# Performance work log

Hardware: AMD Instinct MI355X
Metric: run time of the kernel (lower is better)

The kernel has to match this reference:

```python
import jax, jax.numpy as jnp
import numpy as np

B, S, HID = 2, 2048, 1024
H, D = 16, HID // 16  # heads, head_dim
ROPE_BASE = 10000.0


def setup_inputs() -> dict:
    key = jax.random.key(0)
    k1, k2, k3, k4 = jax.random.split(key, 4)
    scale = 1.0 / np.sqrt(HID)
    return {
        "hidden_states": jax.random.normal(k1, (B, S, HID), dtype=jnp.float32),
        "attention_mask": jnp.zeros((B, 1, 1, S), dtype=jnp.float32),
        "Wq": jax.random.normal(k2, (HID, HID), dtype=jnp.float32) * scale,
        "Wk": jax.random.normal(k3, (HID, HID), dtype=jnp.float32) * scale,
        "Wv": jax.random.normal(k4, (HID, HID), dtype=jnp.float32) * scale,
    }


def _rope_cos_sin(seq_len, dim, dtype):
    inv_freq = 1.0 / (ROPE_BASE ** (jnp.arange(0, dim, 2, dtype=jnp.float32) / dim))
    freqs = jnp.arange(seq_len, dtype=jnp.float32)[:, None] * inv_freq[None, :]  # (S, D/2)
    emb = jnp.concatenate([freqs, freqs], axis=-1)  # (S, D)
    return jnp.cos(emb).astype(dtype), jnp.sin(emb).astype(dtype)


def _rotate_half(x):
    x1, x2 = jnp.split(x, 2, axis=-1)
    return jnp.concatenate([-x2, x1], axis=-1)


def reference(hidden_states, attention_mask, Wq, Wk, Wv):
    b, s, _ = hidden_states.shape
    # QKV projections (no bias), split into heads: (b, H, s, D)
    def proj(W):
        return jnp.einsum('bse,de->bsd', hidden_states, W).reshape(b, s, H, D).transpose(0, 2, 1, 3)
    q, k, v = proj(Wq), proj(Wk), proj(Wv)
    # Rotary embedding on q, k over sequence positions
    cos, sin = _rope_cos_sin(s, D, hidden_states.dtype)  # (s, D)
    cos = cos[None, None]  # (1,1,s,D)
    sin = sin[None, None]
    q = q * cos + _rotate_half(q) * sin
    k = k * cos + _rotate_half(k) * sin
    # Scaled dot-product attention with additive mask
    scores = jnp.einsum('bhqd,bhkd->bhqk', q, k) / jnp.sqrt(jnp.asarray(D, hidden_states.dtype))
    scores = scores + attention_mask
    probs = jax.nn.softmax(scores, axis=-1)  # dropout p=0 (eval) -> identity
    ctx = jnp.einsum('bhqk,bhkd->bhqd', probs, v)
    return ctx.transpose(0, 2, 1, 3).reshape(b, s, H * D)
```

## Files before the change

### kernel.cpp

```cpp
#include <hip/hip_runtime.h>
#include <stdint.h>

typedef unsigned short u16;
typedef short bf16x8 __attribute__((ext_vector_type(8)));
typedef float f32x4 __attribute__((ext_vector_type(4)));

#define S_ 2048
#define HID_ 1024
#define H_ 16
#define D_ 64

#define LOG2E 1.4426950408889634f
#define SCALE_LOG2 0.18033688011112042f
#define MAXC_LOG2 11.541560327111707f

__device__ __forceinline__ u16 f2bf(float f) {
  uint32_t x = __builtin_bit_cast(uint32_t, f);
  uint32_t r = (x + 0x7fffu + ((x >> 16) & 1u)) >> 16;
  return (u16)r;
}
__device__ __forceinline__ uint32_t packbf2(float a, float b) {
  return (uint32_t)f2bf(a) | ((uint32_t)f2bf(b) << 16);
}
__device__ __forceinline__ uint32_t permpack(float a, float b) {
  return __builtin_amdgcn_perm(__builtin_bit_cast(uint32_t, b),
                               __builtin_bit_cast(uint32_t, a), 0x07060302u);
}

__device__ __forceinline__ void gl2lds16(const void* g, void* l) {
  __builtin_amdgcn_global_load_lds(
      (const __attribute__((address_space(1))) unsigned int*)g,
      (__attribute__((address_space(3))) unsigned int*)l, 16, 0, 0);
}

#define NX_ (1 << 20)
#define NW_ (1 << 18)
#define NROPE_ 65536
__global__ void prep_kernel(const float* __restrict__ X, const float* __restrict__ Wq,
                            const float* __restrict__ Wk, const float* __restrict__ Wv,
                            const float* __restrict__ mask, u16* __restrict__ Xb,
                            u16* __restrict__ Wqb, u16* __restrict__ Wkb,
                            u16* __restrict__ Wvb, float* __restrict__ cos_t,
                            float* __restrict__ sin_t, float* __restrict__ mask2) {
  int i = blockIdx.x * 256 + threadIdx.x;
  if (i < NX_ + 3 * NW_) {
    const float* src;
    u16* dst;
    int off;
    if (i < NX_) {
      src = X; dst = Xb; off = i;
    } else if (i < NX_ + NW_) {
      src = Wq; dst = Wqb; off = i - NX_;
    } else if (i < NX_ + 2 * NW_) {
      src = Wk; dst = Wkb; off = i - NX_ - NW_;
    } else {
      src = Wv; dst = Wvb; off = i - NX_ - 2 * NW_;
    }
    float4 v = ((const float4*)src)[off];
    uint2 packed;
    packed.x = packbf2(v.x, v.y);
    packed.y = packbf2(v.z, v.w);
    ((uint2*)dst)[off] = packed;
  } else if (i < NX_ + 3 * NW_ + NROPE_) {
    int t = i - (NX_ + 3 * NW_);
    int s = t >> 5, j = t & 31;
    float invf = powf(10000.0f, -(float)j * (1.0f / 32.0f));
    float ang = (float)s * invf;
    cos_t[t] = cosf(ang);
    sin_t[t] = sinf(ang);
  } else {
    int t = i - (NX_ + 3 * NW_ + NROPE_);
    mask2[t] = fmaf(mask[t], LOG2E, -MAXC_LOG2);
  }
}

__global__ __launch_bounds__(512, 2) void qkv_gemm_kernel(
    const u16* __restrict__ X, const u16* __restrict__ Wq, const u16* __restrict__ Wk,
    const u16* __restrict__ Wv, const float* __restrict__ cos_t,
    const float* __restrict__ sin_t, u16* __restrict__ Q, u16* __restrict__ K,
    u16* __restrict__ Vt) {
  __shared__ char smem[131072];
  int tid = threadIdx.x;
  int lane = tid & 63, wave = tid >> 6;
  int wm = wave >> 2, wn = wave & 3;
  int quad = lane >> 4, l16 = lane & 15;
  int nbase = blockIdx.x * 128;
  int mbase = blockIdx.y * 128;

#define STAGE_ALL(k0, buf)                                                        \
  {                                                                               \
    _Pragma("unroll") for (int it = 0; it < 8; ++it) {                            \
      int j = (it & 1) * 512 + tid;                                               \
      int r = j >> 3, gs = j & 7, gsrc = gs ^ (r & 7);                            \
      const u16* src; int rb;                                                     \
      if ((it >> 1) == 0)      { src = X;  rb = mbase + r; }                      \
      else if ((it >> 1) == 1) { src = Wq; rb = nbase + r; }                      \
      else if ((it >> 1) == 2) { src = Wk; rb = nbase + r; }                      \
      else                     { src = Wv; rb = nbase + r; }                      \
      gl2lds16(src + (size_t)rb * HID_ + (k0) + gsrc * 8,                         \
               (buf) + (it >> 1) * 16384 + j * 16);                               \
    }                                                                             \
  }

  STAGE_ALL(0, smem)

  f32x4 acc[3][4][2] = {};

  for (int kk = 0; kk < 16; ++kk) {
    const char* buf = smem + (kk & 1) * 65536;
    __syncthreads();

    if (kk < 15)
      STAGE_ALL((kk + 1) * 64, smem + ((kk + 1) & 1) * 65536)

#pragma unroll
    for (int kh = 0; kh < 2; ++kh) {
      bf16x8 afrag[4];
#pragma unroll
      for (int i4 = 0; i4 < 4; ++i4) {
        int r = wm * 64 + i4 * 16 + l16;
        int L = r * 8 + ((kh * 4 + quad) ^ (r & 7));
        afrag[i4] = *(const bf16x8*)(buf + L * 16);
      }
#pragma unroll
      for (int w = 0; w < 3; ++w) {
        const char* Bs = buf + 16384 + w * 16384;
        bf16x8 bfrag[2];
#pragma unroll
        for (int j2 = 0; j2 < 2; ++j2) {
          int r = (wn >> 1) * 64 + (wn & 1) * 16 + j2 * 32 + l16;
          int L = r * 8 + ((kh * 4 + quad) ^ (r & 7));
          bfrag[j2] = *(const bf16x8*)(Bs + L * 16);
        }
        if (w == 2) {
#pragma unroll
          for (int i4 = 0; i4 < 4; ++i4)
#pragma unroll
            for (int j2 = 0; j2 < 2; ++j2)
              acc[2][i4][j2] = __builtin_amdgcn_mfma_f32_16x16x32_bf16(
                  afrag[i4], bfrag[j2], acc[2][i4][j2], 0, 0, 0);
        } else if (w == 1) {
#pragma unroll
          for (int i4 = 0; i4 < 4; ++i4)
#pragma unroll
            for (int j2 = 0; j2 < 2; ++j2)
              acc[1][i4][j2] = __builtin_amdgcn_mfma_f32_16x16x32_bf16(
                  bfrag[j2], afrag[i4], acc[1][i4][j2], 0, 0, 0);
        } else {
#pragma unroll
          for (int i4 = 0; i4 < 4; ++i4)
#pragma unroll
            for (int j2 = 0; j2 < 2; ++j2)
              acc[0][i4][j2] = __builtin_amdgcn_mfma_f32_16x16x32_bf16(
                  bfrag[j2], afrag[i4], acc[0][i4][j2], 0, 0, 0);
        }
      }
    }
  }
#undef STAGE_ALL

#pragma unroll
  for (int i4 = 0; i4 < 4; ++i4)
#pragma unroll
    for (int j2 = 0; j2 < 2; ++j2) {
      int m = mbase + wm * 64 + i4 * 16 + quad * 4;
      int n = nbase + (wn >> 1) * 64 + (wn & 1) * 16 + j2 * 32 + l16;
      int b = m >> 11, s0 = m & 2047;
      int h = n >> 6, d = n & 63;
      uint2 pk;
      pk.x = packbf2(acc[2][i4][j2][0], acc[2][i4][j2][1]);
      pk.y = packbf2(acc[2][i4][j2][2], acc[2][i4][j2][3]);
      *(uint2*)(Vt + (((size_t)(b * H_ + h)) * D_ + d) * S_ + s0) = pk;
    }

#pragma unroll
  for (int w = 0; w < 2; ++w) {
    u16* dst = (w == 0) ? Q : K;
#pragma unroll
    for (int i4 = 0; i4 < 4; ++i4) {
      int m = mbase + wm * 64 + i4 * 16 + l16;
      int n1 = nbase + (wn >> 1) * 64 + (wn & 1) * 16 + quad * 4;
      int b = m >> 11, s = m & 2047;
      int h = n1 >> 6, d1 = n1 & 63;
      float4 c4 = *(const float4*)(cos_t + s * 32 + d1);
      float4 s4 = *(const float4*)(sin_t + s * 32 + d1);
      float y1[4], y2[4];
#pragma unroll
      for (int r = 0; r < 4; ++r) {
        float cr = ((const float*)&c4)[r], sr = ((const float*)&s4)[r];
        float x1 = acc[w][i4][0][r], x2 = acc[w][i4][1][r];
        y1[r] = x1 * cr - x2 * sr;
        y2[r] = x2 * cr + x1 * sr;
      }
      size_t base = ((size_t)(b * H_ + h) * S_ + s) * D_;
      uint2 p1, p2;
      p1.x = packbf2(y1[0], y1[1]);
      p1.y = packbf2(y1[2], y1[3]);
      p2.x = packbf2(y2[0], y2[1]);
      p2.y = packbf2(y2[2], y2[3]);
      *(uint2*)(dst + base + d1) = p1;
      *(uint2*)(dst + base + d1 + 32) = p2;
    }
  }
}

__device__ __forceinline__ void softmax_pack(const f32x4 (*s)[4], const float4* mv,
                                             bf16x8 (*pp)[2]) {
#pragma unroll
  for (int qb = 0; qb < 2; ++qb) {
    uint32_t a[4][2];
#pragma unroll
    for (int jt = 0; jt < 4; ++jt) {
      float pf[4];
#pragma unroll
      for (int r = 0; r < 4; ++r) {
        float mvr = ((const float*)&mv[jt])[r];
        pf[r] = __builtin_amdgcn_exp2f(fmaf(s[qb][jt][r], SCALE_LOG2, mvr));
      }
      a[jt][0] = permpack(pf[0], pf[1]);
      a[jt][1] = permpack(pf[2], pf[3]);
    }
#pragma unroll
    for (int kh = 0; kh < 2; ++kh) {
      uint32_t tt[4];
#pragma unroll
      for (int i = 0; i < 2; ++i) {
        auto r1 = __builtin_amdgcn_permlane32_swap(a[2 * kh][i], a[2 * kh + 1][i],
                                                   false, false);
        auto r2 = __builtin_amdgcn_permlane16_swap(r1[0], r1[1], false, false);
        tt[i] = r2[0];
        tt[2 + i] = r2[1];
      }
      union { uint32_t u[4]; bf16x8 v; } cv;
      cv.u[0] = tt[0]; cv.u[1] = tt[1]; cv.u[2] = tt[2]; cv.u[3] = tt[3];
      pp[qb][kh] = cv.v;
    }
  }
}

__global__ __launch_bounds__(256, 2) void flash_kernel(
    const u16* __restrict__ Q, const u16* __restrict__ K, const u16* __restrict__ Vt,
    const float* __restrict__ mask2, float* __restrict__ out) {
  __shared__ char smem[49152];
  int tid = threadIdx.x, wave = tid >> 6;
  int lane = tid & 63;
  int quad = lane >> 4, l16 = lane & 15;
  int bh = blockIdx.y, b = bh >> 4, h = bh & 15;
  int qw = blockIdx.x * 128 + wave * 32;
  const u16* Kbase = K + (size_t)bh * S_ * D_;
  const u16* Vbase = Vt + (size_t)bh * D_ * S_;

  char* bk0 = smem + l16 * 128 + ((quad ^ (l16 & 7)) * 16);
  char* bk1 = smem + l16 * 128 + (((4 + quad) ^ (l16 & 7)) * 16);

  int r0 = tid >> 3, gs = tid & 7, gsrc = gs ^ (r0 & 7);
  size_t koff = (size_t)r0 * D_ + gsrc * 8;
  size_t voff = (size_t)r0 * S_ + gsrc * 8;
  const u16* kg = Kbase;
  const u16* vg = Vbase;
  const float* mq = mask2 + b * S_;

#define STAGE(SB)                                                      \
  {                                                                    \
    gl2lds16(kg + koff, smem + (SB) * 16384 + tid * 16);               \
    gl2lds16(kg + koff + 32 * D_, smem + (SB) * 16384 + 4096 + tid * 16); \
    gl2lds16(vg + voff, smem + (SB) * 16384 + 8192 + tid * 16);        \
    gl2lds16(vg + voff + 32 * S_, smem + (SB) * 16384 + 12288 + tid * 16); \
    kg += 64 * D_;                                                     \
    vg += 64;                                                          \
  }

#define MVLOAD                                                         \
  {                                                                    \
    _Pragma("unroll") for (int jt = 0; jt < 4; ++jt)                   \
        mv[jt] = *(const float4*)(mq + jt * 16 + quad * 4);            \
    mq += 64;                                                          \
  }

#define QK_Z(KOFF, s)                                                             \
  {                                                                               \
    _Pragma("unroll") for (int jt = 0; jt < 4; ++jt) {                            \
      bf16x8 kf0 = *(const bf16x8*)(bk0 + (KOFF) + jt * 2048);                    \
      bf16x8 kf1 = *(const bf16x8*)(bk1 + (KOFF) + jt * 2048);                    \
      s[0][jt] = __builtin_amdgcn_mfma_f32_16x16x32_bf16(kf0, qfrag[0][0], zc, 0, 0, 0); \
      s[0][jt] = __builtin_amdgcn_mfma_f32_16x16x32_bf16(kf1, qfrag[0][1], s[0][jt], 0, 0, 0); \
      s[1][jt] = __builtin_amdgcn_mfma_f32_16x16x32_bf16(kf0, qfrag[1][0], zc, 0, 0, 0); \
      s[1][jt] = __builtin_amdgcn_mfma_f32_16x16x32_bf16(kf1, qfrag[1][1], s[1][jt], 0, 0, 0); \
    }                                                                             \
  }

#define PV(VOFF)                                                                  \
  {                                                                               \
    lacc[0] = __builtin_amdgcn_mfma_f32_16x16x32_bf16(pp[0][0], ones, lacc[0], 0, 0, 0); \
    lacc[0] = __builtin_amdgcn_mfma_f32_16x16x32_bf16(pp[0][1], ones, lacc[0], 0, 0, 0); \
    lacc[1] = __builtin_amdgcn_mfma_f32_16x16x32_bf16(pp[1][0], ones, lacc[1], 0, 0, 0); \
    lacc[1] = __builtin_amdgcn_mfma_f32_16x16x32_bf16(pp[1][1], ones, lacc[1], 0, 0, 0); \
    _Pragma("unroll") for (int jd = 0; jd < 4; ++jd) {                            \
      bf16x8 vf0 = *(const bf16x8*)(bk0 + (VOFF) + jd * 2048);                    \
      bf16x8 vf1 = *(const bf16x8*)(bk1 + (VOFF) + jd * 2048);                    \
      o[0][jd] = __builtin_amdgcn_mfma_f32_16x16x32_bf16(pp[0][0], vf0, o[0][jd], 0, 0, 0); \
      o[0][jd] = __builtin_amdgcn_mfma_f32_16x16x32_bf16(pp[0][1], vf1, o[0][jd], 0, 0, 0); \
      o[1][jd] = __builtin_amdgcn_mfma_f32_16x16x32_bf16(pp[1][0], vf0, o[1][jd], 0, 0, 0); \
      o[1][jd] = __builtin_amdgcn_mfma_f32_16x16x32_bf16(pp[1][1], vf1, o[1][jd], 0, 0, 0); \
    }                                                                             \
  }

#define BODY(M)                                                        \
  {                                                                    \
    __syncthreads();                                                   \
    STAGE(((M) + 1) % 3)                                               \
    __builtin_amdgcn_s_setprio(1);                                     \
    PV((((M) + 2) % 3) * 16384 + 8192)                                 \
    f32x4 s[2][4];                                                     \
    QK_Z((M) * 16384, s)                                               \
    __builtin_amdgcn_s_setprio(0);                                     \
    softmax_pack(s, mv, pp);                                           \
    MVLOAD                                                             \
  }

  bf16x8 qfrag[2][2];
#pragma unroll
  for (int qb = 0; qb < 2; ++qb) {
    const u16* qp = Q + ((size_t)bh * S_ + qw + qb * 16 + l16) * D_ + quad * 8;
    qfrag[qb][0] = *(const bf16x8*)qp;
    qfrag[qb][1] = *(const bf16x8*)(qp + 32);
  }
  bf16x8 ones;
#pragma unroll
  for (int j = 0; j < 8; ++j) ones[j] = (short)0x3f80;
  const f32x4 zc = {0.f, 0.f, 0.f, 0.f};

  f32x4 o[2][4] = {};
  f32x4 lacc[2] = {};
  bf16x8 pp[2][2];
  float4 mv[4];

  STAGE(0)
  MVLOAD

  {
    __syncthreads();
    STAGE(1)
    f32x4 s[2][4];
    __builtin_amdgcn_s_setprio(1);
    QK_Z(0, s)
    __builtin_amdgcn_s_setprio(0);
    softmax_pack(s, mv, pp);
    MVLOAD
  }

  for (int j = 0; j < 10; ++j) {
    BODY(1)
    BODY(2)
    BODY(0)
  }

  {
    __syncthreads();
    __builtin_amdgcn_s_setprio(1);
    PV(0 * 16384 + 8192)
    f32x4 s[2][4];
    QK_Z(1 * 16384, s)
    __builtin_amdgcn_s_setprio(0);
    softmax_pack(s, mv, pp);
  }

  PV(1 * 16384 + 8192)

#undef STAGE
#undef MVLOAD
#undef QK_Z
#undef PV
#undef BODY

  float inv[2][4];
#pragma unroll
  for (int qb = 0; qb < 2; ++qb)
#pragma unroll
    for (int r = 0; r < 4; ++r) inv[qb][r] = 1.0f / lacc[qb][r];
#pragma unroll
  for (int qb = 0; qb < 2; ++qb)
#pragma unroll
    for (int jd = 0; jd < 4; ++jd) {
#pragma unroll
      for (int r = 0; r < 4; ++r) {
        int d = jd * 16 + l16;
        int q = qw + qb * 16 + quad * 4 + r;
        out[(((size_t)b * S_ + q) * H_ + h) * D_ + d] = o[qb][jd][r] * inv[qb][r];
      }
    }
}

extern "C" void kernel_launch(void* const* d_in, const int* in_sizes, int n_in,
                              void* d_out, int out_size, void* d_ws, size_t ws_size,
                              hipStream_t stream) {
  const float* hid = (const float*)d_in[0];
  const float* mask = (const float*)d_in[1];
  const float* Wq = (const float*)d_in[2];
  const float* Wk = (const float*)d_in[3];
  const float* Wv = (const float*)d_in[4];
  float* out = (float*)d_out;
  char* ws = (char*)d_ws;

  u16* Xbf = (u16*)ws;
  u16* Wqb = (u16*)(ws + (8u << 20));
  u16* Wkb = (u16*)(ws + (10u << 20));
  u16* Wvb = (u16*)(ws + (12u << 20));
  u16* Qb = (u16*)(ws + (14u << 20));
  u16* Kb = (u16*)(ws + (22u << 20));
  u16* Vtb = (u16*)(ws + (30u << 20));
  float* cos_t = (float*)(ws + (38u << 20));
  float* sin_t = (float*)(ws + (38u << 20) + (256u << 10));
  float* mask2 = (float*)(ws + (38u << 20) + (512u << 10));

  prep_kernel<<<7440, 256, 0, stream>>>(hid, Wq, Wk, Wv, mask, Xbf, Wqb, Wkb, Wvb,
                                        cos_t, sin_t, mask2);
  qkv_gemm_kernel<<<dim3(8, 32), 512, 0, stream>>>(Xbf, Wqb, Wkb, Wvb, cos_t, sin_t,
                                                   Qb, Kb, Vtb);
  flash_kernel<<<dim3(16, 32), 256, 0, stream>>>(Qb, Kb, Vtb, mask2, out);
}
```

Measured before the change: 157.5 us.

## Restructure QKV GEMM main loop into phased ping-pong schedule with explicit waitcnts

The QKV projection GEMM main loop is split into three phases, one per weight matrix. Each phase loads its LDS fragments, issues half of the next tile's global-to-LDS copies, waits on an explicit vmcnt/lgkmcnt plus a raw s_barrier, then runs its MFMA block at raised wave priority via s_setprio. The goal is to interleave global prefetch with MFMA work and replace the single __syncthreads with finer-grained gates, so memory latency hides behind compute. In exchange there are more barriers per iteration, and correctness depends on hand-tuned vmcnt counts matching the number of issued copies.

```diff
diff --git a/kernel.cpp b/kernel.cpp
--- a/kernel.cpp
+++ b/kernel.cpp
@@ -87,9 +87,9 @@
   int nbase = blockIdx.x * 128;
   int mbase = blockIdx.y * 128;
 
-#define STAGE_ALL(k0, buf)                                                        \
+#define STAGE_HALF(k0, buf, IT0)                                                  \
   {                                                                               \
-    _Pragma("unroll") for (int it = 0; it < 8; ++it) {                            \
+    _Pragma("unroll") for (int it = (IT0); it < (IT0) + 4; ++it) {                \
       int j = (it & 1) * 512 + tid;                                               \
       int r = j >> 3, gs = j & 7, gsrc = gs ^ (r & 7);                            \
       const u16* src; int rb;                                                     \
@@ -102,62 +102,107 @@
     }                                                                             \
   }
 
-  STAGE_ALL(0, smem)
+#define PHASE_GATE                                                     \
+  __builtin_amdgcn_s_barrier();                                        \
+  asm volatile("s_waitcnt lgkmcnt(0)" ::: "memory");                   \
+  __builtin_amdgcn_sched_barrier(0);
+
+  STAGE_HALF(0, smem, 0)
+  STAGE_HALF(0, smem, 4)
+  asm volatile("s_waitcnt vmcnt(0)" ::: "memory");
+  __builtin_amdgcn_s_barrier();
 
   f32x4 acc[3][4][2] = {};
 
   for (int kk = 0; kk < 16; ++kk) {
     const char* buf = smem + (kk & 1) * 65536;
-    __syncthreads();
-
-    if (kk < 15)
-      STAGE_ALL((kk + 1) * 64, smem + ((kk + 1) & 1) * 65536)
-
-#pragma unroll
-    for (int kh = 0; kh < 2; ++kh) {
-      bf16x8 afrag[4];
+    char* nbuf = smem + ((kk + 1) & 1) * 65536;
+    int k0n = (kk + 1) * 64;
+
+    bf16x8 af[2][4], bf[2][2];
+
+#pragma unroll
+    for (int kh = 0; kh < 2; ++kh)
 #pragma unroll
       for (int i4 = 0; i4 < 4; ++i4) {
         int r = wm * 64 + i4 * 16 + l16;
         int L = r * 8 + ((kh * 4 + quad) ^ (r & 7));
-        afrag[i4] = *(const bf16x8*)(buf + L * 16);
-      }
-#pragma unroll
-      for (int w = 0; w < 3; ++w) {
-        const char* Bs = buf + 16384 + w * 16384;
-        bf16x8 bfrag[2];
-#pragma unroll
-        for (int j2 = 0; j2 < 2; ++j2) {
-          int r = (wn >> 1) * 64 + (wn & 1) * 16 + j2 * 32 + l16;
-          int L = r * 8 + ((kh * 4 + quad) ^ (r & 7));
-          bfrag[j2] = *(const bf16x8*)(Bs + L * 16);
-        }
-        if (w == 2) {
-#pragma unroll
-          for (int i4 = 0; i4 < 4; ++i4)
-#pragma unroll
-            for (int j2 = 0; j2 < 2; ++j2)
-              acc[2][i4][j2] = __builtin_amdgcn_mfma_f32_16x16x32_bf16(
-                  afrag[i4], bfrag[j2], acc[2][i4][j2], 0, 0, 0);
-        } else if (w == 1) {
-#pragma unroll
-          for (int i4 = 0; i4 < 4; ++i4)
-#pragma unroll
-            for (int j2 = 0; j2 < 2; ++j2)
-              acc[1][i4][j2] = __builtin_amdgcn_mfma_f32_16x16x32_bf16(
-                  bfrag[j2], afrag[i4], acc[1][i4][j2], 0, 0, 0);
-        } else {
-#pragma unroll
-          for (int i4 = 0; i4 < 4; ++i4)
-#pragma unroll
-            for (int j2 = 0; j2 < 2; ++j2)
-              acc[0][i4][j2] = __builtin_amdgcn_mfma_f32_16x16x32_bf16(
-                  bfrag[j2], afrag[i4], acc[0][i4][j2], 0, 0, 0);
-        }
-      }
-    }
-  }
-#undef STAGE_ALL
+        af[kh][i4] = *(const bf16x8*)(buf + L * 16);
+      }
+#pragma unroll
+    for (int kh = 0; kh < 2; ++kh)
+#pragma unroll
+      for (int j2 = 0; j2 < 2; ++j2) {
+        int r = (wn >> 1) * 64 + (wn & 1) * 16 + j2 * 32 + l16;
+        int L = r * 8 + ((kh * 4 + quad) ^ (r & 7));
+        bf[kh][j2] = *(const bf16x8*)(buf + 16384 + L * 16);
+      }
+    if (kk < 15) {
+      STAGE_HALF(k0n, nbuf, 0)
+      asm volatile("s_waitcnt vmcnt(4)" ::: "memory");
+    } else {
+      asm volatile("s_waitcnt vmcnt(0)" ::: "memory");
+    }
+    PHASE_GATE
+    __builtin_amdgcn_s_setprio(1);
+#pragma unroll
+    for (int kh = 0; kh < 2; ++kh)
+#pragma unroll
+      for (int i4 = 0; i4 < 4; ++i4)
+#pragma unroll
+        for (int j2 = 0; j2 < 2; ++j2)
+          acc[0][i4][j2] = __builtin_amdgcn_mfma_f32_16x16x32_bf16(
+              bf[kh][j2], af[kh][i4], acc[0][i4][j2], 0, 0, 0);
+    __builtin_amdgcn_s_setprio(0);
+    __builtin_amdgcn_s_barrier();
+
+#pragma unroll
+    for (int kh = 0; kh < 2; ++kh)
+#pragma unroll
+      for (int j2 = 0; j2 < 2; ++j2) {
+        int r = (wn >> 1) * 64 + (wn & 1) * 16 + j2 * 32 + l16;
+        int L = r * 8 + ((kh * 4 + quad) ^ (r & 7));
+        bf[kh][j2] = *(const bf16x8*)(buf + 32768 + L * 16);
+      }
+    if (kk < 15) STAGE_HALF(k0n, nbuf, 4)
+    PHASE_GATE
+    __builtin_amdgcn_s_setprio(1);
+#pragma unroll
+    for (int kh = 0; kh < 2; ++kh)
+#pragma unroll
+      for (int i4 = 0; i4 < 4; ++i4)
+#pragma unroll
+        for (int j2 = 0; j2 < 2; ++j2)
+          acc[1][i4][j2] = __builtin_amdgcn_mfma_f32_16x16x32_bf16(
+              bf[kh][j2], af[kh][i4], acc[1][i4][j2], 0, 0, 0);
+    __builtin_amdgcn_s_setprio(0);
+    __builtin_amdgcn_s_barrier();
+
+#pragma unroll
+    for (int kh = 0; kh < 2; ++kh)
+#pragma unroll
+      for (int j2 = 0; j2 < 2; ++j2) {
+        int r = (wn >> 1) * 64 + (wn & 1) * 16 + j2 * 32 + l16;
+        int L = r * 8 + ((kh * 4 + quad) ^ (r & 7));
+        bf[kh][j2] = *(const bf16x8*)(buf + 49152 + L * 16);
+      }
+    if (kk < 15)
+      asm volatile("s_waitcnt vmcnt(4)" ::: "memory");
+    PHASE_GATE
+    __builtin_amdgcn_s_setprio(1);
+#pragma unroll
+    for (int kh = 0; kh < 2; ++kh)
+#pragma unroll
+      for (int i4 = 0; i4 < 4; ++i4)
+#pragma unroll
+        for (int j2 = 0; j2 < 2; ++j2)
+          acc[2][i4][j2] = __builtin_amdgcn_mfma_f32_16x16x32_bf16(
+              af[kh][i4], bf[kh][j2], acc[2][i4][j2], 0, 0, 0);
+    __builtin_amdgcn_s_setprio(0);
+    __builtin_amdgcn_s_barrier();
+  }
+#undef STAGE_HALF
+#undef PHASE_GATE
 
 #pragma unroll
   for (int i4 = 0; i4 < 4; ++i4)
```

New measurement: 159.9 us. Within noise of the previous version (+1.5%).

## Switch flash loop to 128-key tiles with double-buffered LDS

Applied to the files above, without the earlier changes.

Replaces the triple-buffered 64-key pipeline with a double-buffered 128-key pipeline. Each iteration stages two 64-key K/V subtiles, runs two QK+softmax passes, then one PV pass over all 128 keys. This halves the number of barriers and iterations, but LDS grows to 64KB per block, which may limit occupancy at 2 blocks per CU. It also drops the previous software pipelining where PV of the prior tile overlapped QK of the current tile.

```diff
diff --git a/kernel.cpp b/kernel.cpp
--- a/kernel.cpp
+++ b/kernel.cpp
@@ -241,7 +241,7 @@
 __global__ __launch_bounds__(256, 2) void flash_kernel(
     const u16* __restrict__ Q, const u16* __restrict__ K, const u16* __restrict__ Vt,
     const float* __restrict__ mask2, float* __restrict__ out) {
-  __shared__ char smem[49152];
+  __shared__ char smem[65536];
   int tid = threadIdx.x, wave = tid >> 6;
   int lane = tid & 63;
   int quad = lane >> 4, l16 = lane & 15;
@@ -260,62 +260,87 @@
   const u16* vg = Vbase;
   const float* mq = mask2 + b * S_;
 
-#define STAGE(SB)                                                      \
+#define STAGE64(KD, VD)                                                \
   {                                                                    \
-    gl2lds16(kg + koff, smem + (SB) * 16384 + tid * 16);               \
-    gl2lds16(kg + koff + 32 * D_, smem + (SB) * 16384 + 4096 + tid * 16); \
-    gl2lds16(vg + voff, smem + (SB) * 16384 + 8192 + tid * 16);        \
-    gl2lds16(vg + voff + 32 * S_, smem + (SB) * 16384 + 12288 + tid * 16); \
+    gl2lds16(kg + koff, (KD) + tid * 16);                              \
+    gl2lds16(kg + koff + 32 * D_, (KD) + 4096 + tid * 16);             \
+    gl2lds16(vg + voff, (VD) + tid * 16);                              \
+    gl2lds16(vg + voff + 32 * S_, (VD) + 4096 + tid * 16);             \
     kg += 64 * D_;                                                     \
     vg += 64;                                                          \
   }
 
+#define STAGE128(P)                                                    \
+  {                                                                    \
+    STAGE64(smem + (P) * 32768, smem + (P) * 32768 + 16384)            \
+    STAGE64(smem + (P) * 32768 + 8192, smem + (P) * 32768 + 24576)     \
+  }
+
 #define MVLOAD                                                         \
   {                                                                    \
-    _Pragma("unroll") for (int jt = 0; jt < 4; ++jt)                   \
-        mv[jt] = *(const float4*)(mq + jt * 16 + quad * 4);            \
-    mq += 64;                                                          \
-  }
-
-#define QK_Z(KOFF, s)                                                             \
+    _Pragma("unroll") for (int jt = 0; jt < 4; ++jt) {                 \
+      mvA[jt] = *(const float4*)(mq + jt * 16 + quad * 4);             \
+      mvB[jt] = *(const float4*)(mq + 64 + jt * 16 + quad * 4);        \
+    }                                                                  \
+    mq += 128;                                                         \
+  }
+
+#define QKSUB(P, ST, SA)                                                          \
   {                                                                               \
     _Pragma("unroll") for (int jt = 0; jt < 4; ++jt) {                            \
-      bf16x8 kf0 = *(const bf16x8*)(bk0 + (KOFF) + jt * 2048);                    \
-      bf16x8 kf1 = *(const bf16x8*)(bk1 + (KOFF) + jt * 2048);                    \
-      s[0][jt] = __builtin_amdgcn_mfma_f32_16x16x32_bf16(kf0, qfrag[0][0], zc, 0, 0, 0); \
-      s[0][jt] = __builtin_amdgcn_mfma_f32_16x16x32_bf16(kf1, qfrag[0][1], s[0][jt], 0, 0, 0); \
-      s[1][jt] = __builtin_amdgcn_mfma_f32_16x16x32_bf16(kf0, qfrag[1][0], zc, 0, 0, 0); \
-      s[1][jt] = __builtin_amdgcn_mfma_f32_16x16x32_bf16(kf1, qfrag[1][1], s[1][jt], 0, 0, 0); \
+      bf16x8 kf0 = *(const bf16x8*)(bk0 + (P) * 32768 + (ST) * 8192 + jt * 2048); \
+      bf16x8 kf1 = *(const bf16x8*)(bk1 + (P) * 32768 + (ST) * 8192 + jt * 2048); \
+      SA[0][jt] = __builtin_amdgcn_mfma_f32_16x16x32_bf16(kf0, qfrag[0][0], zc, 0, 0, 0); \
+      SA[0][jt] = __builtin_amdgcn_mfma_f32_16x16x32_bf16(kf1, qfrag[0][1], SA[0][jt], 0, 0, 0); \
+      SA[1][jt] = __builtin_amdgcn_mfma_f32_16x16x32_bf16(kf0, qfrag[1][0], zc, 0, 0, 0); \
+      SA[1][jt] = __builtin_amdgcn_mfma_f32_16x16x32_bf16(kf1, qfrag[1][1], SA[1][jt], 0, 0, 0); \
     }                                                                             \
   }
 
-#define PV(VOFF)                                                                  \
+#define PV128(P)                                                                  \
   {                                                                               \
-    lacc[0] = __builtin_amdgcn_mfma_f32_16x16x32_bf16(pp[0][0], ones, lacc[0], 0, 0, 0); \
-    lacc[0] = __builtin_amdgcn_mfma_f32_16x16x32_bf16(pp[0][1], ones, lacc[0], 0, 0, 0); \
-    lacc[1] = __builtin_amdgcn_mfma_f32_16x16x32_bf16(pp[1][0], ones, lacc[1], 0, 0, 0); \
-    lacc[1] = __builtin_amdgcn_mfma_f32_16x16x32_bf16(pp[1][1], ones, lacc[1], 0, 0, 0); \
+    lacc[0] = __builtin_amdgcn_mfma_f32_16x16x32_bf16(ppA[0][0], ones, lacc[0], 0, 0, 0); \
+    lacc[0] = __builtin_amdgcn_mfma_f32_16x16x32_bf16(ppA[0][1], ones, lacc[0], 0, 0, 0); \
+    lacc[0] = __builtin_amdgcn_mfma_f32_16x16x32_bf16(ppB[0][0], ones, lacc[0], 0, 0, 0); \
+    lacc[0] = __builtin_amdgcn_mfma_f32_16x16x32_bf16(ppB[0][1], ones, lacc[0], 0, 0, 0); \
+    lacc[1] = __builtin_amdgcn_mfma_f32_16x16x32_bf16(ppA[1][0], ones, lacc[1], 0, 0, 0); \
+    lacc[1] = __builtin_amdgcn_mfma_f32_16x16x32_bf16(ppA[1][1], ones, lacc[1], 0, 0, 0); \
+    lacc[1] = __builtin_amdgcn_mfma_f32_16x16x32_bf16(ppB[1][0], ones, lacc[1], 0, 0, 0); \
+    lacc[1] = __builtin_amdgcn_mfma_f32_16x16x32_bf16(ppB[1][1], ones, lacc[1], 0, 0, 0); \
     _Pragma("unroll") for (int jd = 0; jd < 4; ++jd) {                            \
-      bf16x8 vf0 = *(const bf16x8*)(bk0 + (VOFF) + jd * 2048);                    \
-      bf16x8 vf1 = *(const bf16x8*)(bk1 + (VOFF) + jd * 2048);                    \
-      o[0][jd] = __builtin_amdgcn_mfma_f32_16x16x32_bf16(pp[0][0], vf0, o[0][jd], 0, 0, 0); \
-      o[0][jd] = __builtin_amdgcn_mfma_f32_16x16x32_bf16(pp[0][1], vf1, o[0][jd], 0, 0, 0); \
-      o[1][jd] = __builtin_amdgcn_mfma_f32_16x16x32_bf16(pp[1][0], vf0, o[1][jd], 0, 0, 0); \
-      o[1][jd] = __builtin_amdgcn_mfma_f32_16x16x32_bf16(pp[1][1], vf1, o[1][jd], 0, 0, 0); \
+      bf16x8 v00 = *(const bf16x8*)(bk0 + (P) * 32768 + 16384 + jd * 2048);       \
+      bf16x8 v01 = *(const bf16x8*)(bk1 + (P) * 32768 + 16384 + jd * 2048);       \
+      bf16x8 v10 = *(const bf16x8*)(bk0 + (P) * 32768 + 24576 + jd * 2048);       \
+      bf16x8 v11 = *(const bf16x8*)(bk1 + (P) * 32768 + 24576 + jd * 2048);       \
+      o[0][jd] = __builtin_amdgcn_mfma_f32_16x16x32_bf16(ppA[0][0], v00, o[0][jd], 0, 0, 0); \
+      o[0][jd] = __builtin_amdgcn_mfma_f32_16x16x32_bf16(ppA[0][1], v01, o[0][jd], 0, 0, 0); \
+      o[0][jd] = __builtin_amdgcn_mfma_f32_16x16x32_bf16(ppB[0][0], v10, o[0][jd], 0, 0, 0); \
+      o[0][jd] = __builtin_amdgcn_mfma_f32_16x16x32_bf16(ppB[0][1], v11, o[0][jd], 0, 0, 0); \
+      o[1][jd] = __builtin_amdgcn_mfma_f32_16x16x32_bf16(ppA[1][0], v00, o[1][jd], 0, 0, 0); \
+      o[1][jd] = __builtin_amdgcn_mfma_f32_16x16x32_bf16(ppA[1][1], v01, o[1][jd], 0, 0, 0); \
+      o[1][jd] = __builtin_amdgcn_mfma_f32_16x16x32_bf16(ppB[1][0], v10, o[1][jd], 0, 0, 0); \
+      o[1][jd] = __builtin_amdgcn_mfma_f32_16x16x32_bf16(ppB[1][1], v11, o[1][jd], 0, 0, 0); \
     }                                                                             \
   }
 
-#define BODY(M)                                                        \
+#define BODY(P)                                                        \
   {                                                                    \
     __syncthreads();                                                   \
-    STAGE(((M) + 1) % 3)                                               \
+    STAGE128((P) ^ 1)                                                  \
     __builtin_amdgcn_s_setprio(1);                                     \
-    PV((((M) + 2) % 3) * 16384 + 8192)                                 \
-    f32x4 s[2][4];                                                     \
-    QK_Z((M) * 16384, s)                                               \
+    f32x4 sS0[2][4];                                                   \
+    QKSUB(P, 0, sS0)                                                   \
     __builtin_amdgcn_s_setprio(0);                                     \
-    softmax_pack(s, mv, pp);                                           \
+    softmax_pack(sS0, mvA, ppA);                                       \
+    __builtin_amdgcn_s_setprio(1);                                     \
+    f32x4 sS1[2][4];                                                   \
+    QKSUB(P, 1, sS1)                                                   \
+    __builtin_amdgcn_s_setprio(0);                                     \
+    softmax_pack(sS1, mvB, ppB);                                       \
     MVLOAD                                                             \
+    __builtin_amdgcn_s_setprio(1);                                     \
+    PV128(P)                                                           \
+    __builtin_amdgcn_s_setprio(0);                                     \
   }
 
   bf16x8 qfrag[2][2];
@@ -332,45 +357,40 @@
 
   f32x4 o[2][4] = {};
   f32x4 lacc[2] = {};
-  bf16x8 pp[2][2];
-  float4 mv[4];
-
-  STAGE(0)
+  bf16x8 ppA[2][2], ppB[2][2];
+  float4 mvA[4], mvB[4];
+
+  STAGE128(0)
   MVLOAD
 
-  {
-    __syncthreads();
-    STAGE(1)
-    f32x4 s[2][4];
-    __builtin_amdgcn_s_setprio(1);
-    QK_Z(0, s)
-    __builtin_amdgcn_s_setprio(0);
-    softmax_pack(s, mv, pp);
-    MVLOAD
-  }
-
-  for (int j = 0; j < 10; ++j) {
+  BODY(0)
+  for (int j = 0; j < 7; ++j) {
     BODY(1)
-    BODY(2)
     BODY(0)
   }
 
   {
     __syncthreads();
     __builtin_amdgcn_s_setprio(1);
-    PV(0 * 16384 + 8192)
-    f32x4 s[2][4];
-    QK_Z(1 * 16384, s)
+    f32x4 sS0[2][4];
+    QKSUB(1, 0, sS0)
     __builtin_amdgcn_s_setprio(0);
-    softmax_pack(s, mv, pp);
-  }
-
-  PV(1 * 16384 + 8192)
-
-#undef STAGE
+    softmax_pack(sS0, mvA, ppA);
+    __builtin_amdgcn_s_setprio(1);
+    f32x4 sS1[2][4];
+    QKSUB(1, 1, sS1)
+    __builtin_amdgcn_s_setprio(0);
+    softmax_pack(sS1, mvB, ppB);
+    __builtin_amdgcn_s_setprio(1);
+    PV128(1)
+    __builtin_amdgcn_s_setprio(0);
+  }
+
+#undef STAGE64
+#undef STAGE128
 #undef MVLOAD
-#undef QK_Z
-#undef PV
+#undef QKSUB
+#undef PV128
 #undef BODY
 
   float inv[2][4];
```

After: 158.2 us. About the same (+0.5%).
